# Kernel tuning notes

Hardware: AMD Instinct MI355X
Metric: run time of the kernel (lower is better)

The kernel has to match this reference:

```python
import jax, jax.numpy as jnp
import numpy as np

# Clause structure: 4 unary clauses and 4 binary (joined-space) clauses,
# each with 3 literals; first literal negated ('n' prefix).
U_IDX = np.array([[0, 1, 2], [3, 4, 5], [6, 7, 8], [9, 10, 11]], dtype=np.int32)
U_SIGNS = np.array([[-1.0, 1.0, 1.0]] * 4, dtype=np.float32)
# Joined matrix columns: [u[i1] (0..15), u[i2] (16..31), binary (32..35)]
B_IDX = np.array([[0, 16, 32], [1, 17, 33], [2, 18, 34], [3, 19, 35]], dtype=np.int32)
B_SIGNS = np.array([[-1.0, 1.0, 1.0]] * 4, dtype=np.float32)

N_NODES, N_UNARY = 50000, 16
N_EDGES, N_BINARY = 1600000, 4
INIT_W = 0.5


def setup_inputs() -> dict:
    key = jax.random.key(0)
    k1, k2, k3, k4 = jax.random.split(key, 4)
    unary = jax.random.normal(k1, (N_NODES, N_UNARY), dtype=jnp.float32)
    binary = jax.random.normal(k2, (N_EDGES, N_BINARY), dtype=jnp.float32)
    edge_index = jax.random.randint(k3, (2, N_EDGES), 0, N_NODES, dtype=jnp.int32)
    wu = jnp.full((4,), INIT_W, dtype=jnp.float32)  # learnable unary clause weights
    wb = jnp.full((4,), INIT_W, dtype=jnp.float32)  # learnable binary clause weights
    return {"unary": unary, "binary": binary, "wu": wu, "wb": wb, "edge_index": edge_index}


def _knowledge_enhancer(x, idx, signs, w):
    """x: [R, P]; idx/signs: [C, L]; w: [C]. Returns summed deltas [R, P]."""
    lit = x[:, idx] * signs                                    # [R, C, L] signed literals
    d = (w[:, None] * jax.nn.softmax(lit, axis=-1)) * signs    # [R, C, L] signed deltas
    return jnp.zeros_like(x).at[:, idx].add(d)                 # scatter-sum over clauses


def reference(unary, binary, wu, wb, edge_index):
    i1, i2 = edge_index[0], edge_index[1]
    P = unary.shape[1]
    # Unary knowledge enhancement
    u = unary + _knowledge_enhancer(unary, U_IDX, U_SIGNS, wu)
    # Join: per-edge [u[i1] | u[i2] | binary]
    joined = jnp.concatenate([u[i1], u[i2], binary], axis=1)   # [E, 2P+B]
    d = _knowledge_enhancer(joined, B_IDX, B_SIGNS, wb)        # [E, 2P+B]
    # GroupBy: scatter node blocks back, keep binary block
    n = unary.shape[0]
    delta_up = (jax.ops.segment_sum(d[:, :P], i1, num_segments=n)
                + jax.ops.segment_sum(d[:, P:2 * P], i2, num_segments=n))
    delta_bp = d[:, 2 * P:]
    # activation = identity (default)
    return u + delta_up, binary + delta_bp
```

## Files before the change

### kernel.cpp

```cpp
#include <hip/hip_runtime.h>
#include <hip/hip_bf16.h>

#define N_NODES 50000
#define N_UNARY 16
#define N_EDGES 1600000
#define N_BINARY 4

typedef float vfloat4 __attribute__((ext_vector_type(4)));

#define FP_SCALE 127.0f
#define FP_INV   (1.0f / 127.0f)

#define BUCKET_SHIFT 11
#define BUCKET_NODES 2048
#define N_BUCKETS 25
#define N_GROUPS 50
#define SEG_CAP 73728
#define N_CHUNKS 10

#define TAILS_STRIDE 16

#define SCAT_BLOCK 1024
#define SCAT_EPT 2
#define SCAT_EDGES (SCAT_BLOCK * SCAT_EPT)
#define SCAT_RECS (2 * SCAT_EDGES)

#define SEG_BYTES   ((size_t)N_GROUPS * SEG_CAP * 8)
#define TAILS_BYTES ((size_t)4096)
#define PART_BYTES  ((size_t)N_GROUPS * N_CHUNKS * BUCKET_NODES * 8)
#define UE_BYTES    ((size_t)N_NODES * 16)
#define WS_NEEDED   (SEG_BYTES + TAILS_BYTES + PART_BYTES + UE_BYTES)

__device__ inline void enhance_u4(const float x[6], float wu0, float wu1,
                                  float u[4]) {
    float l0 = -x[0], l1 = x[1], l2 = x[2];
    float m  = fmaxf(l0, fmaxf(l1, l2));
    float e0 = __expf(l0 - m), e1 = __expf(l1 - m), e2 = __expf(l2 - m);
    float inv = 1.0f / (e0 + e1 + e2);
    u[0] = x[0] - wu0 * e0 * inv;
    u[1] = x[1] + wu0 * e1 * inv;
    u[2] = x[2] + wu0 * e2 * inv;
    float l3 = -x[3], l4 = x[4], l5 = x[5];
    float m2 = fmaxf(l3, fmaxf(l4, l5));
    float f0 = __expf(l3 - m2), f1 = __expf(l4 - m2), f2 = __expf(l5 - m2);
    float inv2 = 1.0f / (f0 + f1 + f2);
    u[3] = x[3] - wu1 * f0 * inv2;
}

__device__ inline void edge_math(const float* unary, const float* binary,
                                 float wu0, float wu1, const float wc[4],
                                 int i1, int i2, int e,
                                 float s0[4], float s1[4],
                                 float* out_b) {
    const float4* u1p = (const float4*)(unary + (size_t)i1 * N_UNARY);
    const float4* u2p = (const float4*)(unary + (size_t)i2 * N_UNARY);
    float4 x1a = u1p[0], x1b = u1p[1];
    float4 x2a = u2p[0], x2b = u2p[1];
    float xa[6] = {x1a.x, x1a.y, x1a.z, x1a.w, x1b.x, x1b.y};
    float xb[6] = {x2a.x, x2a.y, x2a.z, x2a.w, x2b.x, x2b.y};
    float a[4], b[4];
    enhance_u4(xa, wu0, wu1, a);
    enhance_u4(xb, wu0, wu1, b);

    vfloat4 bn = __builtin_nontemporal_load((const vfloat4*)binary + e);
    float bb[4] = {bn.x, bn.y, bn.z, bn.w};
    float ob[4];
#pragma unroll
    for (int c = 0; c < 4; ++c) {
        float l0 = -a[c], l1 = b[c], l2 = bb[c];
        float m  = fmaxf(l0, fmaxf(l1, l2));
        float e0 = __expf(l0 - m);
        float e1 = __expf(l1 - m);
        float e2 = __expf(l2 - m);
        float inv = 1.0f / (e0 + e1 + e2);
        s0[c] = e0 * inv;
        s1[c] = e1 * inv;
        ob[c] = bb[c] + wc[c] * e2 * inv;
    }
    vfloat4 obv = {ob[0], ob[1], ob[2], ob[3]};
    __builtin_nontemporal_store(obv, (vfloat4*)out_b + e);
}

__device__ inline unsigned long long make_rec(const float s[4], int local_id) {
    unsigned v0 = __float2uint_rn(s[0] * FP_SCALE);
    unsigned v1 = __float2uint_rn(s[1] * FP_SCALE);
    unsigned v2 = __float2uint_rn(s[2] * FP_SCALE);
    unsigned v3 = __float2uint_rn(s[3] * FP_SCALE);
    unsigned pl = v0 | (v1 << 7) | (v2 << 14) | (v3 << 21);
    return (unsigned long long)pl | ((unsigned long long)(unsigned)local_id << 28);
}

__device__ inline unsigned long long pack4_16(const float s[4]) {
    unsigned long long a = __float2uint_rn(s[0] * FP_SCALE);
    unsigned long long b = __float2uint_rn(s[1] * FP_SCALE);
    unsigned long long c = __float2uint_rn(s[2] * FP_SCALE);
    unsigned long long d = __float2uint_rn(s[3] * FP_SCALE);
    return a | (b << 16) | (c << 32) | (d << 48);
}

__global__ void __launch_bounds__(256)
kenn_pre_kernel(const float* __restrict__ unary,
                const float* __restrict__ wu,
                float4* __restrict__ ue,
                unsigned* __restrict__ tails) {
    int n = blockIdx.x * blockDim.x + threadIdx.x;
    if (n < N_GROUPS) tails[n * TAILS_STRIDE] = 0u;
    if (n >= N_NODES) return;
    const float4* up = (const float4*)(unary + (size_t)n * N_UNARY);
    float4 x0 = up[0], x1 = up[1];
    float x[6] = {x0.x, x0.y, x0.z, x0.w, x1.x, x1.y};
    float u[4];
    enhance_u4(x, wu[0], wu[1], u);
    ue[n] = make_float4(u[0], u[1], u[2], u[3]);
}

__global__ void __launch_bounds__(SCAT_BLOCK)
kenn_edge_scatter_kernel(const float4* __restrict__ ue,
                         const float* __restrict__ binary,
                         const float* __restrict__ wb,
                         const int* __restrict__ edge_index,
                         unsigned long long* __restrict__ segs,
                         unsigned* __restrict__ tails,
                         float* __restrict__ out_b) {
    __shared__ unsigned l_cnt[N_GROUPS];
    __shared__ unsigned l_pref[N_GROUPS + 1];
    __shared__ unsigned l_gbase[N_GROUPS];
    __shared__ unsigned long long staged[SCAT_RECS];
    __shared__ unsigned char staged_g[SCAT_RECS];

    int tid = threadIdx.x;
    if (tid < N_GROUPS) l_cnt[tid] = 0;
    __syncthreads();

    int base = blockIdx.x * SCAT_EDGES;
    float wc[4] = {wb[0], wb[1], wb[2], wb[3]};

    bool valid[SCAT_EPT];
    int g1[SCAT_EPT], g2[SCAT_EPT];
    unsigned pos1[SCAT_EPT], pos2[SCAT_EPT];
    unsigned long long rec1[SCAT_EPT], rec2[SCAT_EPT];

#pragma unroll
    for (int k = 0; k < SCAT_EPT; ++k) {
        int e = base + k * SCAT_BLOCK + tid;
        valid[k] = (e < N_EDGES);
        if (!valid[k]) continue;
        int i1 = __builtin_nontemporal_load(edge_index + e);
        int i2 = __builtin_nontemporal_load(edge_index + N_EDGES + e);

        float4 av = ue[i1];
        float4 bv = ue[i2];
        float a[4] = {av.x, av.y, av.z, av.w};
        float b[4] = {bv.x, bv.y, bv.z, bv.w};
        vfloat4 bn = __builtin_nontemporal_load((const vfloat4*)binary + e);
        float bb[4] = {bn.x, bn.y, bn.z, bn.w};

        float s0[4], s1[4], ob[4];
#pragma unroll
        for (int c = 0; c < 4; ++c) {
            float l0 = -a[c], l1 = b[c], l2 = bb[c];
            float m  = fmaxf(l0, fmaxf(l1, l2));
            float e0 = __expf(l0 - m);
            float e1 = __expf(l1 - m);
            float e2 = __expf(l2 - m);
            float inv = 1.0f / (e0 + e1 + e2);
            s0[c] = e0 * inv;
            s1[c] = e1 * inv;
            ob[c] = bb[c] + wc[c] * e2 * inv;
        }
        vfloat4 obv = {ob[0], ob[1], ob[2], ob[3]};
        __builtin_nontemporal_store(obv, (vfloat4*)out_b + e);

        rec1[k] = make_rec(s0, i1 & (BUCKET_NODES - 1));
        rec2[k] = make_rec(s1, i2 & (BUCKET_NODES - 1));
        g1[k] = i1 >> BUCKET_SHIFT;
        g2[k] = N_BUCKETS + (i2 >> BUCKET_SHIFT);
        pos1[k] = atomicAdd(&l_cnt[g1[k]], 1u);
        pos2[k] = atomicAdd(&l_cnt[g2[k]], 1u);
    }
    __syncthreads();

    if (tid < 64) {
        unsigned c = (tid < N_GROUPS) ? l_cnt[tid] : 0u;
        unsigned s = c;
#pragma unroll
        for (int off = 1; off < 64; off <<= 1) {
            unsigned o = __shfl_up(s, off, 64);
            if (tid >= off) s += o;
        }
        if (tid < N_GROUPS) l_pref[tid] = s - c;
        if (tid == N_GROUPS - 1) l_pref[N_GROUPS] = s;
    } else if (tid >= 64 && tid < 64 + N_GROUPS) {
        int g = tid - 64;
        unsigned c = l_cnt[g];
        l_gbase[g] = c ? atomicAdd(tails + g * TAILS_STRIDE, c) : 0u;
    }
    __syncthreads();

#pragma unroll
    for (int k = 0; k < SCAT_EPT; ++k) {
        if (!valid[k]) continue;
        unsigned p1 = l_pref[g1[k]] + pos1[k];
        unsigned p2 = l_pref[g2[k]] + pos2[k];
        staged[p1] = rec1[k];  staged_g[p1] = (unsigned char)g1[k];
        staged[p2] = rec2[k];  staged_g[p2] = (unsigned char)g2[k];
    }
    __syncthreads();

    unsigned total = l_pref[N_GROUPS];
    for (unsigned i = tid; i < total; i += SCAT_BLOCK) {
        unsigned g = staged_g[i];
        unsigned long long rec = staged[i];
        unsigned p = l_gbase[g] + (i - l_pref[g]);
        if (p < SEG_CAP)
            __builtin_nontemporal_store(rec, segs + (size_t)g * SEG_CAP + p);
    }
}

__global__ void __launch_bounds__(512)
kenn_reduce_kernel(const unsigned long long* __restrict__ segs,
                   const unsigned* __restrict__ tails,
                   unsigned long long* __restrict__ partials) {
    __shared__ unsigned long long lacc[BUCKET_NODES];
    int chunk = blockIdx.x;
    int g     = blockIdx.y;
    int tid   = threadIdx.x;

    for (int i = tid; i < BUCKET_NODES; i += blockDim.x) lacc[i] = 0ull;
    __syncthreads();

    unsigned cnt = tails[g * TAILS_STRIDE];
    if (cnt > SEG_CAP) cnt = SEG_CAP;
    unsigned csz   = (cnt + N_CHUNKS - 1) / N_CHUNKS;
    unsigned start = chunk * csz;
    unsigned end   = start + csz;
    if (end > cnt) end = cnt;

    const unsigned long long* seg = segs + (size_t)g * SEG_CAP;
    for (unsigned i = start + tid; i < end; i += blockDim.x) {
        unsigned long long r = seg[i];
        unsigned id = (unsigned)(r >> 28) & (BUCKET_NODES - 1);
        unsigned pl = (unsigned)r & 0x0FFFFFFFu;
        unsigned long long exp =
            (unsigned long long)(pl & 127u) |
            ((unsigned long long)(pl & (127u << 7))  << 9)  |
            ((unsigned long long)(pl & (127u << 14)) << 18) |
            ((unsigned long long)(pl & (127u << 21)) << 27);
        atomicAdd(&lacc[id], exp);
    }
    __syncthreads();

    unsigned long long* dst =
        partials + ((size_t)g * N_CHUNKS + chunk) * BUCKET_NODES;
    for (int i = tid; i < BUCKET_NODES; i += blockDim.x)
        __builtin_nontemporal_store(lacc[i], dst + i);
}

__global__ void kenn_node_final_kernel(const float* __restrict__ unary,
                                       const float* __restrict__ wu,
                                       const float* __restrict__ wb,
                                       const unsigned long long* __restrict__ partials,
                                       const unsigned long long* __restrict__ accN,
                                       const unsigned long long* __restrict__ accP,
                                       int use_partials,
                                       float* __restrict__ out_u) {
    int node = blockIdx.x * blockDim.x + threadIdx.x;
    if (node >= N_NODES) return;

    const float4* up = (const float4*)(unary + (size_t)node * N_UNARY);
    float4 x0 = up[0], x1 = up[1], x2 = up[2], x3 = up[3];
    float x[16] = {x0.x, x0.y, x0.z, x0.w,
                   x1.x, x1.y, x1.z, x1.w,
                   x2.x, x2.y, x2.z, x2.w,
                   x3.x, x3.y, x3.z, x3.w};
    float wuc[4] = {wu[0], wu[1], wu[2], wu[3]};

    float y[16];
#pragma unroll
    for (int i = 0; i < 16; ++i) y[i] = x[i];

#pragma unroll
    for (int c = 0; c < 4; ++c) {
        float l0 = -x[3 * c + 0];
        float l1 =  x[3 * c + 1];
        float l2 =  x[3 * c + 2];
        float m  = fmaxf(l0, fmaxf(l1, l2));
        float e0 = __expf(l0 - m);
        float e1 = __expf(l1 - m);
        float e2 = __expf(l2 - m);
        float inv = 1.0f / (e0 + e1 + e2);
        y[3 * c + 0] -= wuc[c] * e0 * inv;
        y[3 * c + 1] += wuc[c] * e1 * inv;
        y[3 * c + 2] += wuc[c] * e2 * inv;
    }

    unsigned long long pn, pp;
    if (use_partials) {
        int bucket = node >> BUCKET_SHIFT;
        int local  = node & (BUCKET_NODES - 1);
        const unsigned long long* pN =
            partials + ((size_t)bucket * N_CHUNKS) * BUCKET_NODES + local;
        const unsigned long long* pP =
            partials + ((size_t)(N_BUCKETS + bucket) * N_CHUNKS) * BUCKET_NODES + local;
        pn = 0ull; pp = 0ull;
#pragma unroll
        for (int c = 0; c < N_CHUNKS; ++c) {
            pn += pN[(size_t)c * BUCKET_NODES];
            pp += pP[(size_t)c * BUCKET_NODES];
        }
    } else {
        pn = accN[node];
        pp = accP[node];
    }

    float wbc[4] = {wb[0], wb[1], wb[2], wb[3]};
    y[0] += wbc[0] * ((float)(int)((pp      ) & 0xffff) - (float)(int)((pn      ) & 0xffff)) * FP_INV;
    y[1] += wbc[1] * ((float)(int)((pp >> 16) & 0xffff) - (float)(int)((pn >> 16) & 0xffff)) * FP_INV;
    y[2] += wbc[2] * ((float)(int)((pp >> 32) & 0xffff) - (float)(int)((pn >> 32) & 0xffff)) * FP_INV;
    y[3] += wbc[3] * ((float)(int)((pp >> 48) & 0xffff) - (float)(int)((pn >> 48) & 0xffff)) * FP_INV;

    float4* op = (float4*)(out_u + (size_t)node * N_UNARY);
    op[0] = make_float4(y[0],  y[1],  y[2],  y[3]);
    op[1] = make_float4(y[4],  y[5],  y[6],  y[7]);
    op[2] = make_float4(y[8],  y[9],  y[10], y[11]);
    op[3] = make_float4(y[12], y[13], y[14], y[15]);
}

__global__ void kenn_edge_atomic_kernel(const float* __restrict__ unary,
                                        const float* __restrict__ binary,
                                        const float* __restrict__ wu,
                                        const float* __restrict__ wb,
                                        const int* __restrict__ edge_index,
                                        unsigned long long* __restrict__ accN,
                                        unsigned long long* __restrict__ accP,
                                        float* __restrict__ out_b) {
    int e = blockIdx.x * blockDim.x + threadIdx.x;
    if (e >= N_EDGES) return;
    int i1 = __builtin_nontemporal_load(edge_index + e);
    int i2 = __builtin_nontemporal_load(edge_index + N_EDGES + e);
    float wu0 = wu[0], wu1 = wu[1];
    float wc[4] = {wb[0], wb[1], wb[2], wb[3]};
    float s0[4], s1[4];
    edge_math(unary, binary, wu0, wu1, wc, i1, i2, e, s0, s1, out_b);
    atomicAdd(accN + i1, pack4_16(s0));
    atomicAdd(accP + i2, pack4_16(s1));
}

extern "C" void kernel_launch(void* const* d_in, const int* in_sizes, int n_in,
                              void* d_out, int out_size, void* d_ws, size_t ws_size,
                              hipStream_t stream) {
    const float* unary      = (const float*)d_in[0];
    const float* binary     = (const float*)d_in[1];
    const float* wu         = (const float*)d_in[2];
    const float* wb         = (const float*)d_in[3];
    const int*   edge_index = (const int*)d_in[4];

    float* out_u = (float*)d_out;
    float* out_b = (float*)d_out + (size_t)N_NODES * N_UNARY;

    if (ws_size >= WS_NEEDED) {
        unsigned long long* segs = (unsigned long long*)d_ws;
        unsigned* tails = (unsigned*)((char*)d_ws + SEG_BYTES);
        unsigned long long* partials =
            (unsigned long long*)((char*)d_ws + SEG_BYTES + TAILS_BYTES);
        float4* ue =
            (float4*)((char*)d_ws + SEG_BYTES + TAILS_BYTES + PART_BYTES);

        {
            dim3 grid((N_NODES + 255) / 256);
            kenn_pre_kernel<<<grid, dim3(256), 0, stream>>>(unary, wu, ue, tails);
        }
        {
            dim3 grid((N_EDGES + SCAT_EDGES - 1) / SCAT_EDGES);
            kenn_edge_scatter_kernel<<<grid, dim3(SCAT_BLOCK), 0, stream>>>(
                ue, binary, wb, edge_index, segs, tails, out_b);
        }
        {
            dim3 grid(N_CHUNKS, N_GROUPS);
            kenn_reduce_kernel<<<grid, dim3(512), 0, stream>>>(
                segs, tails, partials);
        }
        {
            dim3 block(256);
            dim3 grid((N_NODES + 255) / 256);
            kenn_node_final_kernel<<<grid, block, 0, stream>>>(
                unary, wu, wb, partials, nullptr, nullptr, 1, out_u);
        }
    } else {
        unsigned long long* accN = (unsigned long long*)d_ws;
        unsigned long long* accP = accN + N_NODES;
        (void)hipMemsetAsync(accN, 0,
                             (size_t)N_NODES * 2 * sizeof(unsigned long long),
                             stream);
        {
            dim3 block(256);
            dim3 grid((N_EDGES + 255) / 256);
            kenn_edge_atomic_kernel<<<grid, block, 0, stream>>>(
                unary, binary, wu, wb, edge_index, accN, accP, out_b);
        }
        {
            dim3 block(256);
            dim3 grid((N_NODES + 255) / 256);
            kenn_node_final_kernel<<<grid, block, 0, stream>>>(
                unary, wu, wb, nullptr, accN, accP, 0, out_u);
        }
    }
}
```

Before: 144.8 us.

## Replace per-chunk partial buffers with global atomic accumulation and retune scatter block

The reduce kernel now adds its shared-memory bucket sums straight into per-node global accumulators with 64-bit atomics, skipping zero entries. Before, it wrote every chunk's partial array and the final kernel summed ten partials per node. The accumulators are zeroed in the pre kernel, so the final kernel reads one value per node and the partial-buffer traffic is gone. The scatter kernel also moves from 1024 threads with 2 edges each to 512 threads with 4 edges each, sets an occupancy hint, and packs group and position into one register to cut register use. The cost is up to ten atomic contentions per node address.

```diff
diff --git a/kernel.cpp b/kernel.cpp
--- a/kernel.cpp
+++ b/kernel.cpp
@@ -20,16 +20,16 @@
 
 #define TAILS_STRIDE 16
 
-#define SCAT_BLOCK 1024
-#define SCAT_EPT 2
+#define SCAT_BLOCK 512
+#define SCAT_EPT 4
 #define SCAT_EDGES (SCAT_BLOCK * SCAT_EPT)
 #define SCAT_RECS (2 * SCAT_EDGES)
 
 #define SEG_BYTES   ((size_t)N_GROUPS * SEG_CAP * 8)
 #define TAILS_BYTES ((size_t)4096)
-#define PART_BYTES  ((size_t)N_GROUPS * N_CHUNKS * BUCKET_NODES * 8)
+#define ACC_BYTES   ((size_t)N_NODES * 2 * 8)
 #define UE_BYTES    ((size_t)N_NODES * 16)
-#define WS_NEEDED   (SEG_BYTES + TAILS_BYTES + PART_BYTES + UE_BYTES)
+#define WS_NEEDED   (SEG_BYTES + TAILS_BYTES + ACC_BYTES + UE_BYTES)
 
 __device__ inline void enhance_u4(const float x[6], float wu0, float wu1,
                                   float u[4]) {
@@ -102,10 +102,14 @@
 kenn_pre_kernel(const float* __restrict__ unary,
                 const float* __restrict__ wu,
                 float4* __restrict__ ue,
-                unsigned* __restrict__ tails) {
+                unsigned* __restrict__ tails,
+                unsigned long long* __restrict__ accN,
+                unsigned long long* __restrict__ accP) {
     int n = blockIdx.x * blockDim.x + threadIdx.x;
     if (n < N_GROUPS) tails[n * TAILS_STRIDE] = 0u;
     if (n >= N_NODES) return;
+    accN[n] = 0ull;
+    accP[n] = 0ull;
     const float4* up = (const float4*)(unary + (size_t)n * N_UNARY);
     float4 x0 = up[0], x1 = up[1];
     float x[6] = {x0.x, x0.y, x0.z, x0.w, x1.x, x1.y};
@@ -114,7 +118,7 @@
     ue[n] = make_float4(u[0], u[1], u[2], u[3]);
 }
 
-__global__ void __launch_bounds__(SCAT_BLOCK)
+__global__ void __launch_bounds__(SCAT_BLOCK, 8)
 kenn_edge_scatter_kernel(const float4* __restrict__ ue,
                          const float* __restrict__ binary,
                          const float* __restrict__ wb,
@@ -136,8 +140,7 @@
     float wc[4] = {wb[0], wb[1], wb[2], wb[3]};
 
     bool valid[SCAT_EPT];
-    int g1[SCAT_EPT], g2[SCAT_EPT];
-    unsigned pos1[SCAT_EPT], pos2[SCAT_EPT];
+    unsigned posg1[SCAT_EPT], posg2[SCAT_EPT];
     unsigned long long rec1[SCAT_EPT], rec2[SCAT_EPT];
 
 #pragma unroll
@@ -173,10 +176,12 @@
 
         rec1[k] = make_rec(s0, i1 & (BUCKET_NODES - 1));
         rec2[k] = make_rec(s1, i2 & (BUCKET_NODES - 1));
-        g1[k] = i1 >> BUCKET_SHIFT;
-        g2[k] = N_BUCKETS + (i2 >> BUCKET_SHIFT);
-        pos1[k] = atomicAdd(&l_cnt[g1[k]], 1u);
-        pos2[k] = atomicAdd(&l_cnt[g2[k]], 1u);
+        unsigned g1 = (unsigned)(i1 >> BUCKET_SHIFT);
+        unsigned g2 = N_BUCKETS + (unsigned)(i2 >> BUCKET_SHIFT);
+        unsigned p1 = atomicAdd(&l_cnt[g1], 1u);
+        unsigned p2 = atomicAdd(&l_cnt[g2], 1u);
+        posg1[k] = (p1 << 6) | g1;
+        posg2[k] = (p2 << 6) | g2;
     }
     __syncthreads();
 
@@ -200,10 +205,10 @@
 #pragma unroll
     for (int k = 0; k < SCAT_EPT; ++k) {
         if (!valid[k]) continue;
-        unsigned p1 = l_pref[g1[k]] + pos1[k];
-        unsigned p2 = l_pref[g2[k]] + pos2[k];
-        staged[p1] = rec1[k];  staged_g[p1] = (unsigned char)g1[k];
-        staged[p2] = rec2[k];  staged_g[p2] = (unsigned char)g2[k];
+        unsigned g1 = posg1[k] & 63u, p1 = l_pref[g1] + (posg1[k] >> 6);
+        unsigned g2 = posg2[k] & 63u, p2 = l_pref[g2] + (posg2[k] >> 6);
+        staged[p1] = rec1[k];  staged_g[p1] = (unsigned char)g1;
+        staged[p2] = rec2[k];  staged_g[p2] = (unsigned char)g2;
     }
     __syncthreads();
 
@@ -220,7 +225,8 @@
 __global__ void __launch_bounds__(512)
 kenn_reduce_kernel(const unsigned long long* __restrict__ segs,
                    const unsigned* __restrict__ tails,
-                   unsigned long long* __restrict__ partials) {
+                   unsigned long long* __restrict__ accN,
+                   unsigned long long* __restrict__ accP) {
     __shared__ unsigned long long lacc[BUCKET_NODES];
     int chunk = blockIdx.x;
     int g     = blockIdx.y;
@@ -250,19 +256,20 @@
     }
     __syncthreads();
 
-    unsigned long long* dst =
-        partials + ((size_t)g * N_CHUNKS + chunk) * BUCKET_NODES;
-    for (int i = tid; i < BUCKET_NODES; i += blockDim.x)
-        __builtin_nontemporal_store(lacc[i], dst + i);
+    int bucket = (g < N_BUCKETS) ? g : (g - N_BUCKETS);
+    unsigned long long* acc =
+        ((g < N_BUCKETS) ? accN : accP) + (size_t)bucket * BUCKET_NODES;
+    for (int i = tid; i < BUCKET_NODES; i += blockDim.x) {
+        unsigned long long v = lacc[i];
+        if (v) atomicAdd(acc + i, v);
+    }
 }
 
 __global__ void kenn_node_final_kernel(const float* __restrict__ unary,
                                        const float* __restrict__ wu,
                                        const float* __restrict__ wb,
-                                       const unsigned long long* __restrict__ partials,
                                        const unsigned long long* __restrict__ accN,
                                        const unsigned long long* __restrict__ accP,
-                                       int use_partials,
                                        float* __restrict__ out_u) {
     int node = blockIdx.x * blockDim.x + threadIdx.x;
     if (node >= N_NODES) return;
@@ -294,24 +301,8 @@
         y[3 * c + 2] += wuc[c] * e2 * inv;
     }
 
-    unsigned long long pn, pp;
-    if (use_partials) {
-        int bucket = node >> BUCKET_SHIFT;
-        int local  = node & (BUCKET_NODES - 1);
-        const unsigned long long* pN =
-            partials + ((size_t)bucket * N_CHUNKS) * BUCKET_NODES + local;
-        const unsigned long long* pP =
-            partials + ((size_t)(N_BUCKETS + bucket) * N_CHUNKS) * BUCKET_NODES + local;
-        pn = 0ull; pp = 0ull;
-#pragma unroll
-        for (int c = 0; c < N_CHUNKS; ++c) {
-            pn += pN[(size_t)c * BUCKET_NODES];
-            pp += pP[(size_t)c * BUCKET_NODES];
-        }
-    } else {
-        pn = accN[node];
-        pp = accP[node];
-    }
+    unsigned long long pn = accN[node];
+    unsigned long long pp = accP[node];
 
     float wbc[4] = {wb[0], wb[1], wb[2], wb[3]};
     y[0] += wbc[0] * ((float)(int)((pp      ) & 0xffff) - (float)(int)((pn      ) & 0xffff)) * FP_INV;
@@ -361,14 +352,16 @@
     if (ws_size >= WS_NEEDED) {
         unsigned long long* segs = (unsigned long long*)d_ws;
         unsigned* tails = (unsigned*)((char*)d_ws + SEG_BYTES);
-        unsigned long long* partials =
+        unsigned long long* accN =
             (unsigned long long*)((char*)d_ws + SEG_BYTES + TAILS_BYTES);
+        unsigned long long* accP = accN + N_NODES;
         float4* ue =
-            (float4*)((char*)d_ws + SEG_BYTES + TAILS_BYTES + PART_BYTES);
+            (float4*)((char*)d_ws + SEG_BYTES + TAILS_BYTES + ACC_BYTES);
 
         {
             dim3 grid((N_NODES + 255) / 256);
-            kenn_pre_kernel<<<grid, dim3(256), 0, stream>>>(unary, wu, ue, tails);
+            kenn_pre_kernel<<<grid, dim3(256), 0, stream>>>(
+                unary, wu, ue, tails, accN, accP);
         }
         {
             dim3 grid((N_EDGES + SCAT_EDGES - 1) / SCAT_EDGES);
@@ -378,13 +371,13 @@
         {
             dim3 grid(N_CHUNKS, N_GROUPS);
             kenn_reduce_kernel<<<grid, dim3(512), 0, stream>>>(
-                segs, tails, partials);
+                segs, tails, accN, accP);
         }
         {
             dim3 block(256);
             dim3 grid((N_NODES + 255) / 256);
             kenn_node_final_kernel<<<grid, block, 0, stream>>>(
-                unary, wu, wb, partials, nullptr, nullptr, 1, out_u);
+                unary, wu, wb, accN, accP, out_u);
         }
     } else {
         unsigned long long* accN = (unsigned long long*)d_ws;
@@ -402,7 +395,7 @@
             dim3 block(256);
             dim3 grid((N_NODES + 255) / 256);
             kenn_node_final_kernel<<<grid, block, 0, stream>>>(
-                unary, wu, wb, nullptr, accN, accP, 0, out_u);
-        }
-    }
-}
+                unary, wu, wb, accN, accP, out_u);
+        }
+    }
+}
```

Result: slower. 150.7 us (+4.0%).
